# Optimization experiments

Hardware: AMD Instinct MI355X
Metric: run time of the kernel (lower is better)

Reference implementation:

```python
import jax, jax.numpy as jnp
import numpy as np

D_MODEL, D_FF, N_EXPERTS, TOP_K = 1024, 4096, 8, 2

def setup_inputs() -> dict:
    key = jax.random.key(0)
    k1, k2, k3, k4 = jax.random.split(key, 4)
    x = jax.random.normal(k1, (4, 2048, D_MODEL), dtype=jnp.float32)
    # glorot-ish scaled init for weights
    router = jax.random.normal(k2, (D_MODEL, N_EXPERTS), dtype=jnp.float32) * (1.0 / np.sqrt(D_MODEL))
    W1 = jax.random.normal(k3, (N_EXPERTS, D_MODEL, D_FF), dtype=jnp.float32) * (1.0 / np.sqrt(D_MODEL))
    W2 = jax.random.normal(k4, (N_EXPERTS, D_FF, D_MODEL), dtype=jnp.float32) * (1.0 / np.sqrt(D_FF))
    return {"x": x, "router": router, "W1": W1, "W2": W2}

def reference(x, router, W1, W2):
    B, S, d = x.shape
    E = router.shape[1]
    xf = x.reshape(-1, d)                              # [T, d]
    logits = xf @ router                               # [T, E]
    top_v, top_i = jax.lax.top_k(logits, TOP_K)        # [T, k]
    w = jax.nn.softmax(top_v, axis=-1)                 # softmax over selected experts
    # scatter top-k weights into a dense [T, E] gate matrix (indices are distinct)
    gates = jnp.sum(jax.nn.one_hot(top_i, E, dtype=x.dtype) * w[..., None], axis=1)
    out = jnp.zeros_like(xf)
    for e in range(E):                                 # small fixed expert loop
        h = xf @ W1[e]                                 # [T, d_ff]
        h = h * jax.nn.sigmoid(h)                      # swish
        out = out + gates[:, e:e + 1] * (h @ W2[e])    # weighted combine
    return out.reshape(B, S, d)
```

## Files before the change

kernel.cpp:

```cpp
#include <hip/hip_runtime.h>
#include <hip/hip_bf16.h>

#define NTOK 8192
#define DM 1024
#define DFF 4096
#define NE 8
#define MAXT 136

typedef __attribute__((ext_vector_type(8))) short bf16x8;
typedef __attribute__((ext_vector_type(4))) float f32x4;

__device__ __forceinline__ ushort f2bf(float f) {
  __hip_bfloat16 h = __float2bfloat16(f);
  return *reinterpret_cast<ushort*>(&h);
}

__global__ void transpose_cvt(const float* __restrict__ in, ushort* __restrict__ out,
                              int R, int C) {
  __shared__ float t[64][65];
  const float* inp = in + (size_t)blockIdx.z * R * C;
  ushort* op = out + (size_t)blockIdx.z * R * C;
  int c0 = blockIdx.x * 64, r0 = blockIdx.y * 64;
  int tid = threadIdx.x;
#pragma unroll
  for (int it = 0; it < 4; ++it) {
    int r = it * 16 + (tid >> 4);
    int c = (tid & 15) * 4;
    float4 v = *reinterpret_cast<const float4*>(inp + (size_t)(r0 + r) * C + c0 + c);
    t[r][c] = v.x; t[r][c + 1] = v.y; t[r][c + 2] = v.z; t[r][c + 3] = v.w;
  }
  __syncthreads();
  int c = tid >> 2, rc = (tid & 3) * 16;
  union { ushort us[16]; uint4 q[2]; } u;
#pragma unroll
  for (int i = 0; i < 16; ++i) u.us[i] = f2bf(t[rc + i][c]);
  uint4* dst = reinterpret_cast<uint4*>(op + (size_t)(c0 + c) * R + r0 + rc);
  dst[0] = u.q[0];
  dst[1] = u.q[1];
}

__global__ void router_kernel(const float* __restrict__ x, const float* __restrict__ router,
                              int* __restrict__ cnt, int* __restrict__ list,
                              float* __restrict__ wa, ushort* __restrict__ xb) {
  __shared__ float rl[DM * NE];
  int tid = threadIdx.x;
  for (int i = tid; i < DM * NE / 4; i += 256)
    reinterpret_cast<float4*>(rl)[i] = reinterpret_cast<const float4*>(router)[i];
  __syncthreads();
  int wave = tid >> 6, lane = tid & 63;
  int tok0 = blockIdx.x * 32 + wave * 8;
  for (int tI = 0; tI < 8; ++tI) {
    int tok = tok0 + tI;
    float acc[NE];
#pragma unroll
    for (int e2 = 0; e2 < NE; ++e2) acc[e2] = 0.f;
    const float4* xr = reinterpret_cast<const float4*>(x + (size_t)tok * DM);
    ushort xo[16];
#pragma unroll
    for (int c = 0; c < 4; ++c) {
      float4 v = xr[lane * 4 + c];
      int d = lane * 16 + c * 4;
      const float* vv = reinterpret_cast<const float*>(&v);
#pragma unroll
      for (int q = 0; q < 4; ++q) {
        float xv = vv[q];
        xo[c * 4 + q] = f2bf(xv);
#pragma unroll
        for (int e2 = 0; e2 < NE; ++e2) acc[e2] += xv * rl[(d + q) * NE + e2];
      }
    }
    *reinterpret_cast<uint4*>(xb + (size_t)tok * DM + lane * 16) =
        *reinterpret_cast<const uint4*>(&xo[0]);
    *reinterpret_cast<uint4*>(xb + (size_t)tok * DM + lane * 16 + 8) =
        *reinterpret_cast<const uint4*>(&xo[8]);
    for (int off = 32; off > 0; off >>= 1) {
#pragma unroll
      for (int e2 = 0; e2 < NE; ++e2) acc[e2] += __shfl_xor(acc[e2], off, 64);
    }
    if (lane == 0) {
      int i0 = 0; float v0 = acc[0];
#pragma unroll
      for (int e2 = 1; e2 < NE; ++e2) { if (acc[e2] > v0) { v0 = acc[e2]; i0 = e2; } }
      int i1 = -1; float v1 = -3.4e38f;
#pragma unroll
      for (int e2 = 0; e2 < NE; ++e2) { if (e2 != i0 && acc[e2] > v1) { v1 = acc[e2]; i1 = e2; } }
      float e1 = expf(v1 - v0);
      float w0 = 1.f / (1.f + e1);
      float w1 = e1 / (1.f + e1);
      int s0 = atomicAdd(&cnt[i0], 1);
      list[i0 * NTOK + s0] = tok * 2;
      wa[tok * 2] = w0;
      int s1 = atomicAdd(&cnt[i1], 1);
      list[i1 * NTOK + s1] = tok * 2 + 1;
      wa[tok * 2 + 1] = w1;
    }
  }
}

__global__ void build_tiles(const int* __restrict__ cnt, unsigned* __restrict__ table) {
  if (threadIdx.x == 0) {
    int t = 0;
    for (int e = 0; e < NE; ++e) {
      int nt = (cnt[e] + 127) >> 7;
      for (int i = 0; i < nt; ++i) table[t++] = ((unsigned)e << 16) | (unsigned)i;
    }
    for (; t < MAXT; ++t) table[t] = 0xFFFFFFFFu;
  }
}

__device__ __forceinline__ void gl_lds16(unsigned long long g, void* s) {
  __builtin_amdgcn_global_load_lds(
      (const __attribute__((address_space(1))) unsigned int*)g,
      (__attribute__((address_space(3))) unsigned int*)s, 16, 0, 0);
}

#define WAITV0() asm volatile("s_waitcnt vmcnt(0)" ::: "memory")

__device__ __forceinline__ void BARRIER() {
  asm volatile("" ::: "memory");
  __builtin_amdgcn_s_barrier();
  asm volatile("" ::: "memory");
}

template <int PASS, int CPX>
__launch_bounds__(256, 4)
__global__ void moe_gemm(const ushort* __restrict__ Abase,
                         const ushort* __restrict__ Wt,
                         const int* __restrict__ cnt,
                         const int* __restrict__ list,
                         const unsigned* __restrict__ table,
                         const float* __restrict__ wa,
                         ushort* __restrict__ Hbuf,
                         float* __restrict__ out) {
  constexpr int K = (PASS == 1) ? DM : DFF;
  constexpr int NK = K / 64;
  constexpr int NB = (PASS == 1) ? DFF : DM;

  const int bid = blockIdx.x;
  const int xcd = bid & 7;
  const int j = bid >> 3;
  const int c = j / MAXT;
  const int t = j - c * MAXT;
  unsigned td = table[t];
  if (td == 0xFFFFFFFFu) return;
  const int e = td >> 16;
  const int tTile = td & 0xFFFF;
  const int n = cnt[e];
  const int nTile = xcd * CPX + c;

  __shared__ __attribute__((aligned(16))) char As[128 * 128];
  __shared__ __attribute__((aligned(16))) char Bs[128 * 128];
  __shared__ int aL[128];
  __shared__ unsigned long long pL[128];

  const int tid = threadIdx.x;
  if (tid < 128) {
    int slot = tTile * 128 + tid;
    int sl = (slot < n) ? slot : (n - 1);
    int a = list[e * NTOK + sl];
    aL[tid] = (slot < n) ? a : -1;
    size_t row = (PASS == 1) ? (size_t)(a >> 1) : (size_t)a;
    pL[tid] = (unsigned long long)(Abase + row * K);
  }
  __syncthreads();

  const char* WtE = (const char*)(Wt + (size_t)e * NB * K);
  const int sr = tid >> 3;
  const int sc = (tid & 7) * 16;
  unsigned long long sA0[4], sB0[4];
  unsigned dst[4];
#pragma unroll
  for (int jj = 0; jj < 4; ++jj) {
    int row = jj * 32 + sr;
    unsigned swc = (unsigned)(sc ^ ((row & 7) << 4));
    sA0[jj] = pL[row] + swc;
    sB0[jj] = (unsigned long long)WtE + (size_t)(nTile * 128 + row) * (K * 2) + swc;
    dst[jj] = (unsigned)(row * 128 + sc);
  }

  const int wv = tid >> 6, lane = tid & 63;
  const int r0 = (wv >> 1) * 64, c0 = (wv & 1) * 64;

  f32x4 acc[4][4];
#pragma unroll
  for (int m = 0; m < 4; ++m)
#pragma unroll
    for (int nn = 0; nn < 4; ++nn) acc[m][nn] = (f32x4){0.f, 0.f, 0.f, 0.f};

  const int rot = bid & (NK - 1);

  for (int kt = 0; kt < NK; ++kt) {
    int slice = kt + rot;
    if (slice >= NK) slice -= NK;
    const unsigned kbyt = (unsigned)slice << 7;
#pragma unroll
    for (int jj = 0; jj < 4; ++jj) {
      gl_lds16(sA0[jj] + kbyt, As + dst[jj]);
      gl_lds16(sB0[jj] + kbyt, Bs + dst[jj]);
    }
    WAITV0();
    BARRIER();
#pragma unroll
    for (int kk = 0; kk < 2; ++kk) {
      const int kb = kk * 64 + (lane >> 4) * 16;
      bf16x8 af[4], bfr[4];
#pragma unroll
      for (int m = 0; m < 4; ++m) {
        int row = r0 + m * 16 + (lane & 15);
        af[m] = *reinterpret_cast<const bf16x8*>(As + row * 128 + (kb ^ ((row & 7) << 4)));
      }
#pragma unroll
      for (int nn = 0; nn < 4; ++nn) {
        int row = c0 + nn * 16 + (lane & 15);
        bfr[nn] = *reinterpret_cast<const bf16x8*>(Bs + row * 128 + (kb ^ ((row & 7) << 4)));
      }
      __builtin_amdgcn_s_setprio(1);
#pragma unroll
      for (int m = 0; m < 4; ++m)
#pragma unroll
        for (int nn = 0; nn < 4; ++nn)
          acc[m][nn] = __builtin_amdgcn_mfma_f32_16x16x32_bf16(af[m], bfr[nn], acc[m][nn], 0, 0, 0);
      __builtin_amdgcn_s_setprio(0);
    }
    BARRIER();
  }

#pragma unroll
  for (int m = 0; m < 4; ++m) {
#pragma unroll
    for (int jr = 0; jr < 4; ++jr) {
      int lr = r0 + m * 16 + (lane >> 4) * 4 + jr;
      int a = aL[lr];
      if (a < 0) continue;
      if (PASS == 1) {
        ushort* hrow = Hbuf + (size_t)a * DFF + nTile * 128 + c0 + (lane & 15);
#pragma unroll
        for (int nn = 0; nn < 4; ++nn) {
          float v = acc[m][nn][jr];
          hrow[nn * 16] = f2bf(v / (1.f + expf(-v)));
        }
      } else {
        float w = wa[a];
        int tok = a >> 1;
        float* orow = out + (size_t)tok * DM + nTile * 128 + c0 + (lane & 15);
#pragma unroll
        for (int nn = 0; nn < 4; ++nn)
          atomicAdd(&orow[nn * 16], w * acc[m][nn][jr]);
      }
    }
  }
}

extern "C" void kernel_launch(void* const* d_in, const int* in_sizes, int n_in,
                              void* d_out, int out_size, void* d_ws, size_t ws_size,
                              hipStream_t stream) {
  const float* x = (const float*)d_in[0];
  const float* router = (const float*)d_in[1];
  const float* W1 = (const float*)d_in[2];
  const float* W2 = (const float*)d_in[3];
  float* out = (float*)d_out;
  char* ws = (char*)d_ws;

  size_t off = 0;
  ushort* Xb = (ushort*)(ws + off); off += (size_t)NTOK * DM * 2;
  ushort* Wt1 = (ushort*)(ws + off); off += (size_t)NE * DM * DFF * 2;
  ushort* Wt2 = (ushort*)(ws + off); off += (size_t)NE * DM * DFF * 2;
  ushort* H   = (ushort*)(ws + off); off += (size_t)NTOK * 2 * DFF * 2;
  int* cnt  = (int*)(ws + off); off += 256;
  int* list = (int*)(ws + off); off += (size_t)NE * NTOK * 4;
  float* wa = (float*)(ws + off); off += (size_t)NTOK * 2 * 4;
  unsigned* table = (unsigned*)(ws + off); off += MAXT * 4;

  hipMemsetAsync(out, 0, (size_t)NTOK * DM * sizeof(float), stream);
  hipMemsetAsync(cnt, 0, NE * sizeof(int), stream);

  transpose_cvt<<<dim3(DFF / 64, DM / 64, NE), 256, 0, stream>>>(W1, Wt1, DM, DFF);
  transpose_cvt<<<dim3(DM / 64, DFF / 64, NE), 256, 0, stream>>>(W2, Wt2, DFF, DM);
  router_kernel<<<NTOK / 32, 256, 0, stream>>>(x, router, cnt, list, wa, Xb);
  build_tiles<<<1, 64, 0, stream>>>(cnt, table);

  moe_gemm<1, 4><<<8 * 4 * MAXT, 256, 0, stream>>>(Xb, Wt1, cnt, list, table, wa, H, out);
  moe_gemm<2, 1><<<8 * 1 * MAXT, 256, 0, stream>>>(H, Wt2, cnt, list, table, wa, H, out);
}
```

Measured before the change: 760.2 us.

## Pre-pack weights and hidden activations into swizzled contiguous tiles, split-K pass 2

```diff
diff --git a/kernel.cpp b/kernel.cpp
--- a/kernel.cpp
+++ b/kernel.cpp
@@ -15,28 +15,29 @@
   return *reinterpret_cast<ushort*>(&h);
 }
 
-__global__ void transpose_cvt(const float* __restrict__ in, ushort* __restrict__ out,
-                              int R, int C) {
-  __shared__ float t[64][65];
-  const float* inp = in + (size_t)blockIdx.z * R * C;
-  ushort* op = out + (size_t)blockIdx.z * R * C;
-  int c0 = blockIdx.x * 64, r0 = blockIdx.y * 64;
-  int tid = threadIdx.x;
-#pragma unroll
-  for (int it = 0; it < 4; ++it) {
-    int r = it * 16 + (tid >> 4);
-    int c = (tid & 15) * 4;
-    float4 v = *reinterpret_cast<const float4*>(inp + (size_t)(r0 + r) * C + c0 + c);
-    t[r][c] = v.x; t[r][c + 1] = v.y; t[r][c + 2] = v.z; t[r][c + 3] = v.w;
+template <int K, int N>
+__global__ void pack_w(const float* __restrict__ in, ushort* __restrict__ outp) {
+  __shared__ float t[64][129];
+  const int e = blockIdx.z, nT = blockIdx.x, kt = blockIdx.y;
+  const float* src = in + (size_t)e * K * N + (size_t)kt * 64 * N + (size_t)nT * 128;
+  const int tid = threadIdx.x;
+#pragma unroll
+  for (int it = 0; it < 8; ++it) {
+    int idx = it * 256 + tid;
+    int kl = idx >> 5, n4 = idx & 31;
+    float4 v = *reinterpret_cast<const float4*>(src + (size_t)kl * N + n4 * 4);
+    t[kl][n4 * 4 + 0] = v.x; t[kl][n4 * 4 + 1] = v.y;
+    t[kl][n4 * 4 + 2] = v.z; t[kl][n4 * 4 + 3] = v.w;
   }
   __syncthreads();
-  int c = tid >> 2, rc = (tid & 3) * 16;
-  union { ushort us[16]; uint4 q[2]; } u;
-#pragma unroll
-  for (int i = 0; i < 16; ++i) u.us[i] = f2bf(t[rc + i][c]);
-  uint4* dst = reinterpret_cast<uint4*>(op + (size_t)(c0 + c) * R + r0 + rc);
-  dst[0] = u.q[0];
-  dst[1] = u.q[1];
+  const int row = tid >> 1, half = tid & 1;
+  const int s = (row & 7) << 3;
+  union { ushort us[32]; uint4 q[4]; } u;
+#pragma unroll
+  for (int k2 = 0; k2 < 32; ++k2) u.us[k2] = f2bf(t[(half * 32 + k2) ^ s][row]);
+  ushort* dst = outp + ((size_t)(e * (N / 128) + nT) * (K / 64) + kt) * 8192 + row * 64 + half * 32;
+  uint4* d4 = reinterpret_cast<uint4*>(dst);
+  d4[0] = u.q[0]; d4[1] = u.q[1]; d4[2] = u.q[2]; d4[3] = u.q[3];
 }
 
 __global__ void router_kernel(const float* __restrict__ x, const float* __restrict__ router,
@@ -122,60 +123,64 @@
   asm volatile("" ::: "memory");
 }
 
-template <int PASS, int CPX>
+template <int PASS>
 __launch_bounds__(256, 4)
-__global__ void moe_gemm(const ushort* __restrict__ Abase,
-                         const ushort* __restrict__ Wt,
+__global__ void moe_gemm(const ushort* __restrict__ Xb,
+                         const ushort* __restrict__ Wp,
+                         ushort* __restrict__ Hp,
                          const int* __restrict__ cnt,
                          const int* __restrict__ list,
                          const unsigned* __restrict__ table,
                          const float* __restrict__ wa,
-                         ushort* __restrict__ Hbuf,
                          float* __restrict__ out) {
-  constexpr int K = (PASS == 1) ? DM : DFF;
-  constexpr int NK = K / 64;
-  constexpr int NB = (PASS == 1) ? DFF : DM;
+  constexpr int NK = (PASS == 1) ? 16 : 32;
 
   const int bid = blockIdx.x;
   const int xcd = bid & 7;
   const int j = bid >> 3;
-  const int c = j / MAXT;
-  const int t = j - c * MAXT;
+  int t, nTile, kc;
+  if (PASS == 1) { t = j >> 2; nTile = xcd * 4 + (j & 3); kc = 0; }
+  else           { t = j >> 1; nTile = xcd; kc = j & 1; }
   unsigned td = table[t];
   if (td == 0xFFFFFFFFu) return;
   const int e = td >> 16;
   const int tTile = td & 0xFFFF;
   const int n = cnt[e];
-  const int nTile = xcd * CPX + c;
-
-  __shared__ __attribute__((aligned(16))) char As[128 * 128];
-  __shared__ __attribute__((aligned(16))) char Bs[128 * 128];
+
+  __shared__ __attribute__((aligned(16))) char As[16384];
+  __shared__ __attribute__((aligned(16))) char Bs[16384];
   __shared__ int aL[128];
   __shared__ unsigned long long pL[128];
 
   const int tid = threadIdx.x;
-  if (tid < 128) {
-    int slot = tTile * 128 + tid;
-    int sl = (slot < n) ? slot : (n - 1);
-    int a = list[e * NTOK + sl];
-    aL[tid] = (slot < n) ? a : -1;
-    size_t row = (PASS == 1) ? (size_t)(a >> 1) : (size_t)a;
-    pL[tid] = (unsigned long long)(Abase + row * K);
+  if constexpr (PASS == 1) {
+    if (tid < 128) {
+      int slot = tTile * 128 + tid;
+      int sl = (slot < n) ? slot : (n - 1);
+      int a = list[e * NTOK + sl];
+      pL[tid] = (unsigned long long)(Xb + (size_t)(a >> 1) * DM);
+    }
+  } else {
+    if (tid < 128) {
+      int slot = tTile * 128 + tid;
+      aL[tid] = (slot < n) ? list[e * NTOK + slot] : -1;
+    }
   }
   __syncthreads();
 
-  const char* WtE = (const char*)(Wt + (size_t)e * NB * K);
-  const int sr = tid >> 3;
-  const int sc = (tid & 7) * 16;
-  unsigned long long sA0[4], sB0[4];
-  unsigned dst[4];
-#pragma unroll
-  for (int jj = 0; jj < 4; ++jj) {
-    int row = jj * 32 + sr;
-    unsigned swc = (unsigned)(sc ^ ((row & 7) << 4));
-    sA0[jj] = pL[row] + swc;
-    sB0[jj] = (unsigned long long)WtE + (size_t)(nTile * 128 + row) * (K * 2) + swc;
-    dst[jj] = (unsigned)(row * 128 + sc);
+  const char* Bsrc = (const char*)Wp +
+      ((size_t)(e * ((PASS == 1) ? 32 : 8) + nTile) * ((PASS == 1) ? 16 : 64) + kc * 32) * 16384;
+  const char* Asrc = nullptr;
+  unsigned long long sA0[4];
+  if constexpr (PASS == 1) {
+    const int sr = tid >> 3, sc = (tid & 7) * 16;
+#pragma unroll
+    for (int jj = 0; jj < 4; ++jj) {
+      int row = jj * 32 + sr;
+      sA0[jj] = pL[row] + (unsigned)(sc ^ ((row & 7) << 4));
+    }
+  } else {
+    Asrc = (const char*)Hp + ((size_t)t * 64 + kc * 32) * 16384;
   }
 
   const int wv = tid >> 6, lane = tid & 63;
@@ -187,17 +192,21 @@
 #pragma unroll
     for (int nn = 0; nn < 4; ++nn) acc[m][nn] = (f32x4){0.f, 0.f, 0.f, 0.f};
 
-  const int rot = bid & (NK - 1);
-
   for (int kt = 0; kt < NK; ++kt) {
-    int slice = kt + rot;
-    if (slice >= NK) slice -= NK;
-    const unsigned kbyt = (unsigned)slice << 7;
-#pragma unroll
-    for (int jj = 0; jj < 4; ++jj) {
-      gl_lds16(sA0[jj] + kbyt, As + dst[jj]);
-      gl_lds16(sB0[jj] + kbyt, Bs + dst[jj]);
-    }
+    if constexpr (PASS == 1) {
+#pragma unroll
+      for (int jj = 0; jj < 4; ++jj)
+        gl_lds16(sA0[jj] + (unsigned)kt * 128, As + jj * 4096 + tid * 16);
+    } else {
+#pragma unroll
+      for (int jj = 0; jj < 4; ++jj)
+        gl_lds16((unsigned long long)(Asrc + (size_t)kt * 16384 + jj * 4096 + tid * 16),
+                 As + jj * 4096 + tid * 16);
+    }
+#pragma unroll
+    for (int jj = 0; jj < 4; ++jj)
+      gl_lds16((unsigned long long)(Bsrc + (size_t)kt * 16384 + jj * 4096 + tid * 16),
+               Bs + jj * 4096 + tid * 16);
     WAITV0();
     BARRIER();
 #pragma unroll
@@ -230,16 +239,18 @@
 #pragma unroll
     for (int jr = 0; jr < 4; ++jr) {
       int lr = r0 + m * 16 + (lane >> 4) * 4 + jr;
-      int a = aL[lr];
-      if (a < 0) continue;
-      if (PASS == 1) {
-        ushort* hrow = Hbuf + (size_t)a * DFF + nTile * 128 + c0 + (lane & 15);
+      if constexpr (PASS == 1) {
 #pragma unroll
         for (int nn = 0; nn < 4; ++nn) {
+          int cg = nTile * 128 + c0 + nn * 16 + (lane & 15);
           float v = acc[m][nn][jr];
-          hrow[nn * 16] = f2bf(v / (1.f + expf(-v)));
+          size_t us = ((size_t)t * 64 + (cg >> 6)) * 8192 + (size_t)lr * 64 +
+                      ((cg & 63) ^ ((lr & 7) << 3));
+          Hp[us] = f2bf(v / (1.f + expf(-v)));
         }
       } else {
+        int a = aL[lr];
+        if (a < 0) continue;
         float w = wa[a];
         int tok = a >> 1;
         float* orow = out + (size_t)tok * DM + nTile * 128 + c0 + (lane & 15);
@@ -261,11 +272,11 @@
   float* out = (float*)d_out;
   char* ws = (char*)d_ws;
 
-  size_t off = 0;
-  ushort* Xb = (ushort*)(ws + off); off += (size_t)NTOK * DM * 2;
-  ushort* Wt1 = (ushort*)(ws + off); off += (size_t)NE * DM * DFF * 2;
-  ushort* Wt2 = (ushort*)(ws + off); off += (size_t)NE * DM * DFF * 2;
-  ushort* H   = (ushort*)(ws + off); off += (size_t)NTOK * 2 * DFF * 2;
+  ushort* Xb  = (ushort*)(ws + 0);
+  ushort* Wp1 = (ushort*)(ws + (size_t)16 * 1024 * 1024);
+  ushort* Wp2 = (ushort*)(ws + 0);
+  size_t off = (size_t)80 * 1024 * 1024;
+  ushort* Hp = (ushort*)(ws + off); off += (size_t)MAXT * 64 * 16384;
   int* cnt  = (int*)(ws + off); off += 256;
   int* list = (int*)(ws + off); off += (size_t)NE * NTOK * 4;
   float* wa = (float*)(ws + off); off += (size_t)NTOK * 2 * 4;
@@ -274,11 +285,13 @@
   hipMemsetAsync(out, 0, (size_t)NTOK * DM * sizeof(float), stream);
   hipMemsetAsync(cnt, 0, NE * sizeof(int), stream);
 
-  transpose_cvt<<<dim3(DFF / 64, DM / 64, NE), 256, 0, stream>>>(W1, Wt1, DM, DFF);
-  transpose_cvt<<<dim3(DM / 64, DFF / 64, NE), 256, 0, stream>>>(W2, Wt2, DFF, DM);
+  pack_w<DM, DFF><<<dim3(DFF / 128, DM / 64, NE), 256, 0, stream>>>(W1, Wp1);
   router_kernel<<<NTOK / 32, 256, 0, stream>>>(x, router, cnt, list, wa, Xb);
   build_tiles<<<1, 64, 0, stream>>>(cnt, table);
 
-  moe_gemm<1, 4><<<8 * 4 * MAXT, 256, 0, stream>>>(Xb, Wt1, cnt, list, table, wa, H, out);
-  moe_gemm<2, 1><<<8 * 1 * MAXT, 256, 0, stream>>>(H, Wt2, cnt, list, table, wa, H, out);
-}
+  moe_gemm<1><<<8 * 4 * MAXT, 256, 0, stream>>>(Xb, Wp1, Hp, cnt, list, table, wa, out);
+
+  pack_w<DFF, DM><<<dim3(DM / 128, DFF / 64, NE), 256, 0, stream>>>(W2, Wp2);
+
+  moe_gemm<2><<<8 * 2 * MAXT, 256, 0, stream>>>(Xb, Wp2, Hp, cnt, list, table, wa, out);
+}
```

New measurement: 675.2 us. -11.2%, faster.
